# Kernel optimization log

Measured on AMD Instinct MI355X. Metric: run time of the kernel, lower is better.

Reference implementation:

```python
import jax, jax.numpy as jnp
import numpy as np

B, N, M = 4, 8192, 2048
D_POINTS, D_MODEL, K = 128, 256, 16


def _linear_params(key, fan_in, fan_out, bias=True):
    kw, kb = jax.random.split(key)
    s = 1.0 / np.sqrt(fan_in)
    W = jax.random.uniform(kw, (fan_in, fan_out), jnp.float32, -s, s)
    if bias:
        b = jax.random.uniform(kb, (fan_out,), jnp.float32, -s, s)
        return W, b
    return W


def setup_inputs() -> dict:
    key = jax.random.key(0)
    ks = jax.random.split(key, 16)
    xyz = jax.random.normal(ks[0], (B, N, 3), jnp.float32)
    features = jax.random.normal(ks[1], (B, N, D_POINTS), jnp.float32)
    query = jax.random.normal(ks[2], (B, M, 3 + D_POINTS), jnp.float32)
    fc1_w, fc1_b = _linear_params(ks[3], D_POINTS, D_MODEL)
    fc2_w, fc2_b = _linear_params(ks[4], D_MODEL, D_POINTS)
    d1_w, d1_b = _linear_params(ks[5], 3, D_MODEL)
    d2_w, d2_b = _linear_params(ks[6], D_MODEL, D_MODEL)
    g1_w, g1_b = _linear_params(ks[7], D_MODEL, D_MODEL)
    g2_w, g2_b = _linear_params(ks[8], D_MODEL, D_MODEL)
    wq = _linear_params(ks[9], D_POINTS, D_MODEL, bias=False)
    wk = _linear_params(ks[10], D_MODEL, D_MODEL, bias=False)
    wv = _linear_params(ks[11], D_MODEL, D_MODEL, bias=False)
    return dict(xyz=xyz, features=features, query=query,
                fc1_w=fc1_w, fc1_b=fc1_b, fc2_w=fc2_w, fc2_b=fc2_b,
                d1_w=d1_w, d1_b=d1_b, d2_w=d2_w, d2_b=d2_b,
                g1_w=g1_w, g1_b=g1_b, g2_w=g2_w, g2_b=g2_b,
                wq=wq, wk=wk, wv=wv, k=K)


def reference(xyz, features, query, fc1_w, fc1_b, fc2_w, fc2_b,
              d1_w, d1_b, d2_w, d2_b, g1_w, g1_b, g2_w, g2_b,
              wq, wk, wv, k):
    query_xyz = query[:, :, :3]            # [B,M,3]
    query_f = query[:, :, 3:]              # [B,M,d_points]

    # KNN: squared distances query_xyz -> xyz, take k smallest
    q2 = jnp.sum(query_xyz * query_xyz, axis=-1)          # [B,M]
    x2 = jnp.sum(xyz * xyz, axis=-1)                      # [B,N]
    cross = jnp.einsum('bmd,bnd->bmn', query_xyz, xyz)    # [B,M,N]
    dist = q2[:, :, None] + x2[:, None, :] - 2.0 * cross
    _, knn_idx = jax.lax.top_k(-dist, k)                  # [B,M,K]

    knn_xyz = jnp.take_along_axis(xyz[:, None], knn_idx[..., None], axis=2)       # [B,M,K,3]
    knn_features = jnp.take_along_axis(features[:, None], knn_idx[..., None], axis=2)  # [B,M,K,d_points]

    q = query_f @ wq                                      # [B,M,d_model]
    x = knn_features @ fc1_w + fc1_b                      # [B,M,K,d_model]
    k_mat = x @ wk
    v = x @ wv

    # positional encoding MLP on coordinate deltas
    delta = query_xyz[:, :, None, :] - knn_xyz            # [B,M,K,3]
    pos_enc = jax.nn.relu(delta @ d1_w + d1_b) @ d2_w + d2_b

    # subtraction-based attention with per-channel softmax over neighbors
    a = q[:, :, None, :] - k_mat + pos_enc
    attn = jax.nn.relu(a @ g1_w + g1_b) @ g2_w + g2_b
    attn = jax.nn.softmax(attn / np.sqrt(k_mat.shape[-1]), axis=-2)

    res = jnp.einsum('bmnf,bmnf->bmf', attn, v + pos_enc)
    res = res @ fc2_w + fc2_b + query_f                   # [B,M,d_points]
    return res, attn
```

## Files before the change

kernel.cpp:

```cpp
#include <hip/hip_runtime.h>
#include <cstdint>
#include <cstddef>

#define BB 4
#define NN 8192
#define MM 2048
#define KK 16
#define DP 128
#define DM 256
#define QROW 131
#define KNQ 2
#define CAP2 384

typedef __attribute__((ext_vector_type(8))) short short8;
typedef __attribute__((ext_vector_type(4))) float floatx4;

__device__ __forceinline__ unsigned short f2bf(float x) {
  unsigned u = __float_as_uint(x);
  unsigned r = (u + 0x7FFFu + ((u >> 16) & 1u)) >> 16;
  return (unsigned short)r;
}

__device__ __forceinline__ unsigned dkey(float qx, float qy, float qz, float q2,
                                         float xx, float xy, float xz, float x2) {
  float cr = fmaf(qz, xz, fmaf(qy, xy, qx * xx));
  float d  = fmaf(-2.0f, cr, q2 + x2);
  unsigned u = __float_as_uint(d);
  return (u & 0x80000000u) ? ~u : (u | 0x80000000u);
}

__global__ __launch_bounds__(256) void prep_weights(
    const float* __restrict__ wq, const float* __restrict__ fc1,
    const float* __restrict__ wk, const float* __restrict__ wv,
    const float* __restrict__ d2, const float* __restrict__ g1,
    const float* __restrict__ g2, const float* __restrict__ fc2,
    unsigned short* __restrict__ dst)
{
  long e = (long)blockIdx.x * 256 + threadIdx.x;
  if (e >= 425984) return;
  const float* src; int sh; int Nmat; long off; bool neg = false;
  if (e < 32768)       { src = wq;  sh = 7; Nmat = 256; off = 0; }
  else if (e < 65536)  { src = fc1; sh = 7; Nmat = 256; off = 32768; }
  else if (e < 131072) { src = wk;  sh = 8; Nmat = 256; off = 65536; neg = true; }
  else if (e < 196608) { src = wv;  sh = 8; Nmat = 256; off = 131072; }
  else if (e < 262144) { src = d2;  sh = 8; Nmat = 256; off = 196608; }
  else if (e < 327680) { src = g1;  sh = 8; Nmat = 256; off = 262144; }
  else if (e < 393216) { src = g2;  sh = 8; Nmat = 256; off = 327680; }
  else                 { src = fc2; sh = 8; Nmat = 128; off = 393216; }
  long d = e - off;
  int K = 1 << sh;
  int n = (int)(d >> sh), k = (int)(d & (K - 1));
  float v = src[(long)k * Nmat + n];
  dst[e] = f2bf(neg ? -v : v);
}

__global__ __launch_bounds__(128) void knn_kernel(
    const float* __restrict__ xyz, const float* __restrict__ query,
    int* __restrict__ knn_out)
{
  __shared__ unsigned long long cand[KNQ][CAP2];
  __shared__ int s_cnt[KNQ];

  const int tid = threadIdx.x;
  const int l = tid & 63, w = tid >> 6;
  const int bmw = blockIdx.x * KNQ + w;
  const int b = bmw >> 11;
  const float* X = xyz + (size_t)b * NN * 3;
  const float* qp = query + (size_t)bmw * QROW;
  const float qx = qp[0], qy = qp[1], qz = qp[2];
  const float q2 = fmaf(qz, qz, fmaf(qy, qy, qx * qx));

  if (l == 0) s_cnt[w] = 0;

  unsigned sk[16];
  #pragma unroll
  for (int i = 0; i < 16; ++i) {
    int n = i * 64 + l;
    float xx = X[3*n], xy = X[3*n + 1], xz = X[3*n + 2];
    float x2 = fmaf(xz, xz, fmaf(xy, xy, xx * xx));
    sk[i] = dkey(qx, qy, qz, q2, xx, xy, xz, x2);
  }
  unsigned T = 0xFFFFFFFFu;
  for (int r = 0; r < KK; ++r) {
    unsigned m = sk[0];
    #pragma unroll
    for (int i = 1; i < 16; ++i) m = sk[i] < m ? sk[i] : m;
    #pragma unroll
    for (int d = 32; d >= 1; d >>= 1) {
      unsigned o = __shfl_xor(m, d, 64);
      m = o < m ? o : m;
    }
    T = m;
    #pragma unroll
    for (int i = 0; i < 16; ++i) if (sk[i] == m) sk[i] = 0xFFFFFFFFu;
  }

  for (int n = l; n < NN; n += 64) {
    float xx = X[3*n], xy = X[3*n + 1], xz = X[3*n + 2];
    float x2 = fmaf(xz, xz, fmaf(xy, xy, xx * xx));
    unsigned u = dkey(qx, qy, qz, q2, xx, xy, xz, x2);
    if (u <= T) {
      int p = atomicAdd(&s_cnt[w], 1);
      if (p < CAP2) cand[w][p] = ((unsigned long long)u << 32) | (unsigned)n;
    }
  }
  const int cnt = s_cnt[w];

  if (cnt <= CAP2) {
    unsigned long long v[CAP2 / 64];
    #pragma unroll
    for (int i = 0; i < CAP2/64; ++i) {
      int p = i*64 + l;
      v[i] = (p < cnt) ? cand[w][p] : ~0ull;
    }
    for (int r = 0; r < KK; ++r) {
      unsigned long long m = v[0];
      #pragma unroll
      for (int i = 1; i < CAP2/64; ++i) m = v[i] < m ? v[i] : m;
      #pragma unroll
      for (int d = 32; d >= 1; d >>= 1) {
        unsigned long long o = __shfl_xor(m, d, 64);
        m = o < m ? o : m;
      }
      if (l == 0) knn_out[bmw*KK + r] = (int)(unsigned)(m & 0xffffffffu);
      #pragma unroll
      for (int i = 0; i < CAP2/64; ++i) if (v[i] == m) v[i] = ~0ull;
    }
  } else {
    unsigned long long last = 0;
    for (int r = 0; r < KK; ++r) {
      unsigned long long best = ~0ull;
      for (int n = l; n < NN; n += 64) {
        float xx = X[3*n], xy = X[3*n + 1], xz = X[3*n + 2];
        float x2 = fmaf(xz, xz, fmaf(xy, xy, xx * xx));
        unsigned u = dkey(qx, qy, qz, q2, xx, xy, xz, x2);
        unsigned long long comp = ((unsigned long long)u << 32) | (unsigned)n;
        if (comp > last && comp < best) best = comp;
      }
      #pragma unroll
      for (int d = 32; d >= 1; d >>= 1) {
        unsigned long long o = __shfl_xor(best, d, 64);
        best = o < best ? o : best;
      }
      last = best;
      if (l == 0) knn_out[bmw*KK + r] = (int)(unsigned)(best & 0xffffffffu);
    }
  }
}

template<int KT, int RT>
__device__ __forceinline__ void gemm_tiles(
    const unsigned short* aBase, int aStride,
    const unsigned short* __restrict__ bT,
    int lm, int lq, int colBase, int rtBase, floatx4 (&acc)[RT][4])
{
  const unsigned short* aRow = aBase + (rtBase*16 + lm)*aStride + lq*8;
  const unsigned short* bRow = bT + (size_t)(colBase + lm)*(KT*32) + lq*8;
  #pragma unroll 2
  for (int ks = 0; ks < KT; ++ks) {
    short8 af[RT];
    #pragma unroll
    for (int rt = 0; rt < RT; ++rt)
      af[rt] = *(const short8*)&aRow[rt*16*aStride + ks*32];
    short8 bf[4];
    #pragma unroll
    for (int c = 0; c < 4; ++c)
      bf[c] = *(const short8*)&bRow[(size_t)c*16*(KT*32) + ks*32];
    #pragma unroll
    for (int rt = 0; rt < RT; ++rt)
      #pragma unroll
      for (int c = 0; c < 4; ++c)
        acc[rt][c] = __builtin_amdgcn_mfma_f32_16x16x32_bf16(af[rt], bf[c], acc[rt][c], 0, 0, 0);
  }
}

__global__ __launch_bounds__(256, 2) void fused_mfma(
    const float* __restrict__ xyz, const float* __restrict__ features,
    const float* __restrict__ query,
    const float* __restrict__ fc1_b, const float* __restrict__ fc2_b,
    const float* __restrict__ d1_w,  const float* __restrict__ d1_b,
    const float* __restrict__ d2_b,
    const float* __restrict__ g1_b,  const float* __restrict__ g2_b,
    const unsigned short* __restrict__ wT,
    const int* __restrict__ knn_idx,
    float* __restrict__ out_res, float* __restrict__ out_attn)
{
  const unsigned short* wq_t  = wT;
  const unsigned short* fc1_t = wT + 32768;
  const unsigned short* wkN_t = wT + 65536;
  const unsigned short* wv_t  = wT + 131072;
  const unsigned short* d2_t  = wT + 196608;
  const unsigned short* g1_t  = wT + 262144;
  const unsigned short* g2_t  = wT + 327680;
  const unsigned short* fc2_t = wT + 393216;

  __shared__ alignas(16) unsigned short bufA[64*264];
  __shared__ alignas(16) unsigned short bufB[64*264];
  __shared__ alignas(16) unsigned short s_qf[16*136];
  __shared__ alignas(16) float s_q[4*256];
  __shared__ float s_delta[64][4];
  __shared__ int   s_idx[64];

  const int tid = threadIdx.x;
  const int l  = tid & 63, w = tid >> 6;
  const int lm = l & 15,  lq = l >> 4;
  const int colBase = w * 64;
  const int bm0 = blockIdx.x << 2;
  const int b   = bm0 >> 11;

  if (tid < 64) {
    int q = tid >> 4, n = tid & 15;
    int idx = knn_idx[(bm0 + q)*KK + n];
    s_idx[tid] = idx;
    const float* qp = query + (size_t)(bm0 + q) * QROW;
    const float* xp = xyz + ((size_t)b*NN + idx)*3;
    s_delta[tid][0] = qp[0] - xp[0];
    s_delta[tid][1] = qp[1] - xp[1];
    s_delta[tid][2] = qp[2] - xp[2];
  }
  {
    int e = tid * 2;
    int q = e >> 7, c = e & 127;
    const float* qp = query + (size_t)(bm0 + q)*QROW + 3 + c;
    unsigned v = ((unsigned)f2bf(qp[1]) << 16) | f2bf(qp[0]);
    *(unsigned*)&s_qf[q*136 + c] = v;
  }
  __syncthreads();
  {
    int r = tid >> 2, c0 = (tid & 3) * 32;
    const float4* fp4 = (const float4*)(features + ((size_t)b*NN + s_idx[r])*DP + c0);
    unsigned short* dst = &bufA[r*136 + c0];
    #pragma unroll
    for (int i = 0; i < 8; ++i) {
      float4 v4 = fp4[i];
      *(unsigned*)&dst[i*4]     = ((unsigned)f2bf(v4.y) << 16) | f2bf(v4.x);
      *(unsigned*)&dst[i*4 + 2] = ((unsigned)f2bf(v4.w) << 16) | f2bf(v4.z);
    }
  }
  __syncthreads();

  const floatx4 zero4 = {0.f, 0.f, 0.f, 0.f};

  {
    floatx4 acc[4][4];
    #pragma unroll
    for (int rt = 0; rt < 4; ++rt)
      #pragma unroll
      for (int c = 0; c < 4; ++c) acc[rt][c] = zero4;
    gemm_tiles<4,4>(bufA, 136, fc1_t, lm, lq, colBase, 0, acc);
    #pragma unroll
    for (int c = 0; c < 4; ++c) {
      float bias = fc1_b[colBase + c*16 + lm];
      #pragma unroll
      for (int rt = 0; rt < 4; ++rt)
        #pragma unroll
        for (int r = 0; r < 4; ++r)
          bufB[(rt*16 + lq*4 + r)*264 + colBase + c*16 + lm] = f2bf(acc[rt][c][r] + bias);
    }
  }
  {
    floatx4 qa[1][4];
    #pragma unroll
    for (int c = 0; c < 4; ++c) qa[0][c] = zero4;
    gemm_tiles<4,1>(s_qf, 136, wq_t, lm, lq, colBase, 0, qa);
    if (lq == 0) {
      #pragma unroll
      for (int c = 0; c < 4; ++c)
        #pragma unroll
        for (int r = 0; r < 4; ++r)
          s_q[r*256 + colBase + c*16 + lm] = qa[0][c][r];
    }
  }
  __syncthreads();

  {
    int c = tid;
    float w0 = d1_w[c], w1 = d1_w[256 + c], w2 = d1_w[512 + c], bb = d1_b[c];
    #pragma unroll 4
    for (int r = 0; r < 64; ++r) {
      float v = fmaf(s_delta[r][2], w2, fmaf(s_delta[r][1], w1,
                fmaf(s_delta[r][0], w0, bb)));
      bufA[r*264 + c] = f2bf(v > 0.f ? v : 0.f);
    }
  }
  __syncthreads();

  floatx4 pe[4][4];
  #pragma unroll
  for (int rt = 0; rt < 4; ++rt)
    #pragma unroll
    for (int c = 0; c < 4; ++c) pe[rt][c] = zero4;
  gemm_tiles<8,4>(bufA, 264, d2_t, lm, lq, colBase, 0, pe);
  #pragma unroll
  for (int c = 0; c < 4; ++c) {
    float bias = d2_b[colBase + c*16 + lm];
    #pragma unroll
    for (int rt = 0; rt < 4; ++rt)
      #pragma unroll
      for (int r = 0; r < 4; ++r) pe[rt][c][r] += bias;
  }

  floatx4 vpe[4][4];
  #pragma unroll
  for (int rt = 0; rt < 4; ++rt)
    #pragma unroll
    for (int c = 0; c < 4; ++c) vpe[rt][c] = pe[rt][c];
  gemm_tiles<8,4>(bufB, 264, wv_t, lm, lq, colBase, 0, vpe);
  __syncthreads();

  {
    floatx4 acc[4][4];
    #pragma unroll
    for (int rt = 0; rt < 4; ++rt)
      #pragma unroll
      for (int c = 0; c < 4; ++c) {
        float qv = s_q[rt*256 + colBase + c*16 + lm];
        #pragma unroll
        for (int r = 0; r < 4; ++r) acc[rt][c][r] = qv + pe[rt][c][r];
      }
    gemm_tiles<8,4>(bufB, 264, wkN_t, lm, lq, colBase, 0, acc);
    #pragma unroll
    for (int rt = 0; rt < 4; ++rt)
      #pragma unroll
      for (int c = 0; c < 4; ++c)
        #pragma unroll
        for (int r = 0; r < 4; ++r)
          bufA[(rt*16 + lq*4 + r)*264 + colBase + c*16 + lm] = f2bf(acc[rt][c][r]);
  }
  __syncthreads();

  {
    floatx4 h[4][4];
    #pragma unroll
    for (int rt = 0; rt < 4; ++rt)
      #pragma unroll
      for (int c = 0; c < 4; ++c) h[rt][c] = zero4;
    gemm_tiles<8,4>(bufA, 264, g1_t, lm, lq, colBase, 0, h);
    #pragma unroll
    for (int c = 0; c < 4; ++c) {
      float bias = g1_b[colBase + c*16 + lm];
      #pragma unroll
      for (int rt = 0; rt < 4; ++rt)
        #pragma unroll
        for (int r = 0; r < 4; ++r) {
          float v = h[rt][c][r] + bias;
          bufB[(rt*16 + lq*4 + r)*264 + colBase + c*16 + lm] = f2bf(v > 0.f ? v : 0.f);
        }
    }
  }
  __syncthreads();

  unsigned short* s_rm = bufA;
  {
    floatx4 lg[4][4];
    #pragma unroll
    for (int rt = 0; rt < 4; ++rt)
      #pragma unroll
      for (int c = 0; c < 4; ++c) lg[rt][c] = zero4;
    gemm_tiles<8,4>(bufB, 264, g2_t, lm, lq, colBase, 0, lg);
    #pragma unroll
    for (int rt = 0; rt < 4; ++rt) {
      #pragma unroll
      for (int c = 0; c < 4; ++c) {
        float bias = g2_b[colBase + c*16 + lm];
        float v[4];
        float mx = -INFINITY;
        #pragma unroll
        for (int r = 0; r < 4; ++r) {
          v[r] = (lg[rt][c][r] + bias) * 0.0625f;
          mx = fmaxf(mx, v[r]);
        }
        mx = fmaxf(mx, __shfl_xor(mx, 16, 64));
        mx = fmaxf(mx, __shfl_xor(mx, 32, 64));
        float s = 0.f;
        #pragma unroll
        for (int r = 0; r < 4; ++r) { v[r] = __expf(v[r] - mx); s += v[r]; }
        s += __shfl_xor(s, 16, 64);
        s += __shfl_xor(s, 32, 64);
        float inv = 1.0f / s;
        float rm = 0.f;
        size_t abase = ((size_t)(bm0 + rt)*KK)*DM + colBase + c*16 + lm;
        #pragma unroll
        for (int r = 0; r < 4; ++r) {
          float at = v[r] * inv;
          __builtin_nontemporal_store(at, &out_attn[abase + (size_t)(lq*4 + r)*DM]);
          rm = fmaf(at, vpe[rt][c][r], rm);
        }
        rm += __shfl_xor(rm, 16, 64);
        rm += __shfl_xor(rm, 32, 64);
        if (lq == 0) s_rm[rt*264 + colBase + c*16 + lm] = f2bf(rm);
      }
    }
  }
  __syncthreads();

  {
    floatx4 acc[2];
    acc[0] = zero4; acc[1] = zero4;
    #pragma unroll 2
    for (int ks = 0; ks < 8; ++ks) {
      short8 af = *(const short8*)&s_rm[lm*264 + ks*32 + lq*8];
      #pragma unroll
      for (int c = 0; c < 2; ++c) {
        int col = (w*2 + c)*16 + lm;
        short8 bf = *(const short8*)&fc2_t[(size_t)col*256 + ks*32 + lq*8];
        acc[c] = __builtin_amdgcn_mfma_f32_16x16x32_bf16(af, bf, acc[c], 0, 0, 0);
      }
    }
    if (lq == 0) {
      #pragma unroll
      for (int c = 0; c < 2; ++c) {
        int col = (w*2 + c)*16 + lm;
        float bias = fc2_b[col];
        #pragma unroll
        for (int r = 0; r < 4; ++r) {
          float res = acc[c][r] + bias + query[(size_t)(bm0 + r)*QROW + 3 + col];
          __builtin_nontemporal_store(res, &out_res[(size_t)(bm0 + r)*DP + col]);
        }
      }
    }
  }
}

extern "C" void kernel_launch(void* const* d_in, const int* in_sizes, int n_in,
                              void* d_out, int out_size, void* d_ws, size_t ws_size,
                              hipStream_t stream) {
  const float* xyz      = (const float*)d_in[0];
  const float* features = (const float*)d_in[1];
  const float* query    = (const float*)d_in[2];
  const float* fc1_w    = (const float*)d_in[3];
  const float* fc1_b    = (const float*)d_in[4];
  const float* fc2_w    = (const float*)d_in[5];
  const float* fc2_b    = (const float*)d_in[6];
  const float* d1_w     = (const float*)d_in[7];
  const float* d1_b     = (const float*)d_in[8];
  const float* d2_w     = (const float*)d_in[9];
  const float* d2_b     = (const float*)d_in[10];
  const float* g1_w     = (const float*)d_in[11];
  const float* g1_b     = (const float*)d_in[12];
  const float* g2_w     = (const float*)d_in[13];
  const float* g2_b     = (const float*)d_in[14];
  const float* wq       = (const float*)d_in[15];
  const float* wk       = (const float*)d_in[16];
  const float* wv       = (const float*)d_in[17];

  int* knn = (int*)d_ws;
  unsigned short* wT = (unsigned short*)((char*)d_ws + 524288);
  float* out_res  = (float*)d_out;
  float* out_attn = (float*)d_out + (size_t)BB*MM*DP;

  prep_weights<<<1664, 256, 0, stream>>>(wq, fc1_w, wk, wv, d2_w, g1_w, g2_w, fc2_w, wT);
  knn_kernel<<<BB*MM/KNQ, 128, 0, stream>>>(xyz, query, knn);
  fused_mfma<<<BB*MM/4, 256, 0, stream>>>(
      xyz, features, query, fc1_b, fc2_b, d1_w, d1_b, d2_b, g1_b, g2_b,
      wT, knn, out_res, out_attn);
}
```

Before: 552.7 us.

## Replace threshold-and-filter KNN with per-lane sorted top-16 insertion over two queries

The KNN kernel drops its two-pass scheme (estimate a threshold from a sample, atomically collect candidates into shared memory, then select, with a brute-force fallback). Instead each lane keeps a register-resident sorted list of 16 candidates for each of two queries, streams the points with vectorized float4 loads, and merges the lists at the end with wave shuffles. This removes the second pass over xyz, the shared-memory atomics and the fallback path, and reuses each point load for two queries. In exchange each lane carries 32 64-bit registers for the lists and pays a branchy insertion step whenever any lane holds a better candidate, which may be costly early in the scan.

After: 826.6 us. 1.5x slower.

```diff
diff --git a/kernel.cpp b/kernel.cpp
--- a/kernel.cpp
+++ b/kernel.cpp
@@ -9,8 +9,6 @@
 #define DP 128
 #define DM 256
 #define QROW 131
-#define KNQ 2
-#define CAP2 384
 
 typedef __attribute__((ext_vector_type(8))) short short8;
 typedef __attribute__((ext_vector_type(4))) float floatx4;
@@ -54,96 +52,77 @@
   dst[e] = f2bf(neg ? -v : v);
 }
 
-__global__ __launch_bounds__(128) void knn_kernel(
+__device__ __forceinline__ void ins16(unsigned long long (&t)[16],
+                                      unsigned long long c) {
+  if (__any(c < t[15])) {
+    #pragma unroll
+    for (int j = 15; j >= 1; --j)
+      t[j] = (c < t[j-1]) ? t[j-1] : ((c < t[j]) ? c : t[j]);
+    t[0] = (c < t[0]) ? c : t[0];
+  }
+}
+
+__global__ __launch_bounds__(256, 4) void knn_kernel(
     const float* __restrict__ xyz, const float* __restrict__ query,
     int* __restrict__ knn_out)
 {
-  __shared__ unsigned long long cand[KNQ][CAP2];
-  __shared__ int s_cnt[KNQ];
-
   const int tid = threadIdx.x;
   const int l = tid & 63, w = tid >> 6;
-  const int bmw = blockIdx.x * KNQ + w;
-  const int b = bmw >> 11;
+  const int qbase = (blockIdx.x * 4 + w) * 2;
+  const int b = qbase >> 11;
   const float* X = xyz + (size_t)b * NN * 3;
-  const float* qp = query + (size_t)bmw * QROW;
-  const float qx = qp[0], qy = qp[1], qz = qp[2];
-  const float q2 = fmaf(qz, qz, fmaf(qy, qy, qx * qx));
-
-  if (l == 0) s_cnt[w] = 0;
-
-  unsigned sk[16];
-  #pragma unroll
-  for (int i = 0; i < 16; ++i) {
-    int n = i * 64 + l;
-    float xx = X[3*n], xy = X[3*n + 1], xz = X[3*n + 2];
-    float x2 = fmaf(xz, xz, fmaf(xy, xy, xx * xx));
-    sk[i] = dkey(qx, qy, qz, q2, xx, xy, xz, x2);
-  }
-  unsigned T = 0xFFFFFFFFu;
-  for (int r = 0; r < KK; ++r) {
-    unsigned m = sk[0];
-    #pragma unroll
-    for (int i = 1; i < 16; ++i) m = sk[i] < m ? sk[i] : m;
-    #pragma unroll
-    for (int d = 32; d >= 1; d >>= 1) {
-      unsigned o = __shfl_xor(m, d, 64);
-      m = o < m ? o : m;
-    }
-    T = m;
-    #pragma unroll
-    for (int i = 0; i < 16; ++i) if (sk[i] == m) sk[i] = 0xFFFFFFFFu;
-  }
-
-  for (int n = l; n < NN; n += 64) {
-    float xx = X[3*n], xy = X[3*n + 1], xz = X[3*n + 2];
-    float x2 = fmaf(xz, xz, fmaf(xy, xy, xx * xx));
-    unsigned u = dkey(qx, qy, qz, q2, xx, xy, xz, x2);
-    if (u <= T) {
-      int p = atomicAdd(&s_cnt[w], 1);
-      if (p < CAP2) cand[w][p] = ((unsigned long long)u << 32) | (unsigned)n;
-    }
-  }
-  const int cnt = s_cnt[w];
-
-  if (cnt <= CAP2) {
-    unsigned long long v[CAP2 / 64];
-    #pragma unroll
-    for (int i = 0; i < CAP2/64; ++i) {
-      int p = i*64 + l;
-      v[i] = (p < cnt) ? cand[w][p] : ~0ull;
-    }
+
+  float qx[2], qy[2], qz[2], q2[2];
+  #pragma unroll
+  for (int q = 0; q < 2; ++q) {
+    const float* qp = query + (size_t)(qbase + q) * QROW;
+    qx[q] = qp[0]; qy[q] = qp[1]; qz[q] = qp[2];
+    q2[q] = fmaf(qz[q], qz[q], fmaf(qy[q], qy[q], qx[q] * qx[q]));
+  }
+
+  unsigned long long t0[16], t1[16];
+  #pragma unroll
+  for (int i = 0; i < 16; ++i) { t0[i] = ~0ull; t1[i] = ~0ull; }
+
+  for (int it = 0; it < NN / 256; ++it) {
+    int p0 = it * 256 + l * 4;
+    const float4* P = (const float4*)(X + 3 * p0);
+    float4 A = P[0], Bv = P[1], C = P[2];
+    float px[4] = {A.x, A.w, Bv.z, C.y};
+    float py[4] = {A.y, Bv.x, Bv.w, C.z};
+    float pz[4] = {A.z, Bv.y, C.x, C.w};
+    #pragma unroll
+    for (int j = 0; j < 4; ++j) {
+      float x2 = fmaf(pz[j], pz[j], fmaf(py[j], py[j], px[j] * px[j]));
+      unsigned idx = (unsigned)(p0 + j);
+      unsigned u0 = dkey(qx[0], qy[0], qz[0], q2[0], px[j], py[j], pz[j], x2);
+      ins16(t0, ((unsigned long long)u0 << 32) | idx);
+      unsigned u1 = dkey(qx[1], qy[1], qz[1], q2[1], px[j], py[j], pz[j], x2);
+      ins16(t1, ((unsigned long long)u1 << 32) | idx);
+    }
+  }
+
+  #pragma unroll
+  for (int q = 0; q < 2; ++q) {
     for (int r = 0; r < KK; ++r) {
-      unsigned long long m = v[0];
-      #pragma unroll
-      for (int i = 1; i < CAP2/64; ++i) m = v[i] < m ? v[i] : m;
+      unsigned long long m = q == 0 ? t0[0] : t1[0];
       #pragma unroll
       for (int d = 32; d >= 1; d >>= 1) {
         unsigned long long o = __shfl_xor(m, d, 64);
         m = o < m ? o : m;
       }
-      if (l == 0) knn_out[bmw*KK + r] = (int)(unsigned)(m & 0xffffffffu);
-      #pragma unroll
-      for (int i = 0; i < CAP2/64; ++i) if (v[i] == m) v[i] = ~0ull;
-    }
-  } else {
-    unsigned long long last = 0;
-    for (int r = 0; r < KK; ++r) {
-      unsigned long long best = ~0ull;
-      for (int n = l; n < NN; n += 64) {
-        float xx = X[3*n], xy = X[3*n + 1], xz = X[3*n + 2];
-        float x2 = fmaf(xz, xz, fmaf(xy, xy, xx * xx));
-        unsigned u = dkey(qx, qy, qz, q2, xx, xy, xz, x2);
-        unsigned long long comp = ((unsigned long long)u << 32) | (unsigned)n;
-        if (comp > last && comp < best) best = comp;
-      }
-      #pragma unroll
-      for (int d = 32; d >= 1; d >>= 1) {
-        unsigned long long o = __shfl_xor(best, d, 64);
-        best = o < best ? o : best;
-      }
-      last = best;
-      if (l == 0) knn_out[bmw*KK + r] = (int)(unsigned)(best & 0xffffffffu);
+      if (l == 0) knn_out[(qbase + q) * KK + r] = (int)(unsigned)(m & 0xffffffffu);
+      if (q == 0) {
+        bool own = (t0[0] == m);
+        #pragma unroll
+        for (int j = 0; j < 15; ++j) t0[j] = own ? t0[j+1] : t0[j];
+        if (own) t0[15] = ~0ull;
+      } else {
+        bool own = (t1[0] == m);
+        #pragma unroll
+        for (int j = 0; j < 15; ++j) t1[j] = own ? t1[j+1] : t1[j];
+        if (own) t1[15] = ~0ull;
+      }
     }
   }
 }
@@ -450,7 +429,7 @@
   float* out_attn = (float*)d_out + (size_t)BB*MM*DP;
 
   prep_weights<<<1664, 256, 0, stream>>>(wq, fc1_w, wk, wv, d2_w, g1_w, g2_w, fc2_w, wT);
-  knn_kernel<<<BB*MM/KNQ, 128, 0, stream>>>(xyz, query, knn);
+  knn_kernel<<<1024, 256, 0, stream>>>(xyz, query, knn);
   fused_mfma<<<BB*MM/4, 256, 0, stream>>>(
       xyz, features, query, fc1_b, fc2_b, d1_w, d1_b, d2_b, g1_b, g2_b,
       wT, knn, out_res, out_attn);
```
